# Performance work log

Hardware: AMD Instinct MI355X
Metric: run time of the kernel (lower is better)

Reference implementation:

```python
import jax, jax.numpy as jnp
import numpy as np

EPS = 1e-9
NUM_GATES = 64
SECOND_THRESHOLD = 0.2  # eval threshold (module defaults train==eval)
CAPACITY_FACTOR = 1.25
MIN_EXPERT_CAPACITY = 4


def setup_inputs() -> dict:
    key = jax.random.key(0)
    k1, k2, k3 = jax.random.split(key, 3)
    b, n, d = 8, 2048, 1024
    x = jax.random.normal(k1, (b, n, d), dtype=jnp.float32)
    w_gating = jax.random.normal(k2, (d, NUM_GATES), dtype=jnp.float32)
    uniform_noise = jax.random.uniform(k3, (b, n), dtype=jnp.float32)
    return {"x": x, "w_gating": w_gating, "uniform_noise": uniform_noise}


def reference(x, w_gating, uniform_noise):
    b, n, d = x.shape
    e = NUM_GATES
    dt = x.dtype

    # raw gates: small matmul + softmax over experts
    raw_gates = jax.nn.softmax(jnp.einsum('bnd,de->bne', x, w_gating), axis=-1)

    # top-1 expert
    gate_1 = jnp.max(raw_gates, axis=-1)            # [b, n]
    index_1 = jnp.argmax(raw_gates, axis=-1)        # [b, n]
    mask_1 = jax.nn.one_hot(index_1, e, dtype=dt)   # [b, n, e]
    density_1_proxy = raw_gates

    # top-2 expert (top-1 of gates with top-1 removed)
    gates_wo1 = raw_gates * (1.0 - mask_1)
    gate_2 = jnp.max(gates_wo1, axis=-1)
    index_2 = jnp.argmax(gates_wo1, axis=-1)
    mask_2 = jax.nn.one_hot(index_2, e, dtype=dt)

    # renormalize top-2 gate values
    denom = gate_1 + gate_2 + EPS
    gate_1 = gate_1 / denom
    gate_2 = gate_2 / denom

    # load-balancing loss
    density_1 = jnp.mean(mask_1, axis=-2)                 # [b, e]
    loss = jnp.mean(jnp.mean(density_1_proxy, axis=-2) * density_1) * float(e * e)

    # second policy == 'random': route to 2nd expert with prob ~ gate_2 / threshold
    keep2 = (uniform_noise < (gate_2 / max(SECOND_THRESHOLD, EPS))).astype(dt)
    mask_2 = mask_2 * keep2[..., None]

    # static expert capacity
    cap = max(min(n, int((n * 2) / e * CAPACITY_FACTOR)), MIN_EXPERT_CAPACITY)
    capf = float(cap)

    # exclusive cumsum over tokens -> position of each token within its expert
    pos1 = (jnp.cumsum(mask_1, axis=-2) - mask_1) * mask_1        # [b, n, e]
    mask_1 = mask_1 * (pos1 < capf).astype(dt)
    mask_1_count = jnp.sum(mask_1, axis=-2, keepdims=True)        # [b, 1, e]
    mask_1_flat = jnp.sum(mask_1, axis=-1)                        # [b, n]
    pos1 = jnpp_sum = jnp.sum(pos1, axis=-1)                      # [b, n]
    gate_1 = gate_1 * mask_1_flat

    pos2 = (jnp.cumsum(mask_2, axis=-2) - mask_2) + mask_1_count
    pos2 = pos2 * mask_2
    mask_2 = mask_2 * (pos2 < capf).astype(dt)
    mask_2_flat = jnp.sum(mask_2, axis=-1)
    pos2 = jnp.sum(pos2, axis=-1)
    gate_2 = gate_2 * mask_2_flat

    # combine tensor [b, n, e, cap]; out-of-range positions one-hot to zero
    oh_e1 = jax.nn.one_hot(index_1, e, dtype=dt)
    oh_e2 = jax.nn.one_hot(index_2, e, dtype=dt)
    oh_c1 = jax.nn.one_hot(pos1.astype(jnp.int32), cap, dtype=dt)
    oh_c2 = jax.nn.one_hot(pos2.astype(jnp.int32), cap, dtype=dt)
    combine = (gate_1[..., None, None] * oh_e1[..., :, None] * oh_c1[..., None, :]
               + gate_2[..., None, None] * oh_e2[..., :, None] * oh_c2[..., None, :])
    dispatch = (combine > 0).astype(dt)
    return dispatch, combine, loss
```

## Files before the change

kernel.cpp:

```cpp
#include <hip/hip_runtime.h>
#include <math.h>

#define NTOK 16384
#define NPB  2048
#define DDIM 1024
#define NEXP 64
#define CAP  80
#define ROWF 5120
#define SOUT 83886080LL

typedef float vf4 __attribute__((ext_vector_type(4)));

#define OFF_ROUTE  0
#define OFF_POS1   (OFF_ROUTE + NTOK*4)
#define OFF_POS2   (OFF_POS1  + NTOK*4)
#define OFF_CNT1   (OFF_POS2  + NTOK*4)
#define OFF_PART   (OFF_CNT1  + 2048)
#define OFF_G12    (OFF_PART  + 65536)

__global__ __launch_bounds__(256) void k_gate(
    const float* __restrict__ x, const float* __restrict__ w,
    const float* __restrict__ noise,
    int* __restrict__ route, float2* __restrict__ g12,
    float* __restrict__ part)
{
    __shared__ float xs[32][68];
    __shared__ float wl[32][64];
    __shared__ float lg[64][68];
    __shared__ float sG[4][64];

    const int tid  = threadIdx.x;
    const int tok0 = blockIdx.x * 64;
    const int tx = tid & 15, ty = tid >> 4;
    float acc[4][4] = {{0.f}};

    const float* xb = x + (size_t)tok0 * DDIM;
    const int t0 = tid >> 3, c0 = (tid & 7) * 4;

    float4 px0 = *(const float4*)(xb + (size_t)t0 * DDIM + c0);
    float4 px1 = *(const float4*)(xb + (size_t)(t0 + 32) * DDIM + c0);
    float4 pw0 = ((const float4*)w)[tid];
    float4 pw1 = ((const float4*)w)[tid + 256];

    for (int k0 = 0; k0 < DDIM; k0 += 32) {
        xs[c0+0][t0] = px0.x; xs[c0+1][t0] = px0.y;
        xs[c0+2][t0] = px0.z; xs[c0+3][t0] = px0.w;
        xs[c0+0][t0+32] = px1.x; xs[c0+1][t0+32] = px1.y;
        xs[c0+2][t0+32] = px1.z; xs[c0+3][t0+32] = px1.w;
        ((float4*)wl)[tid]       = pw0;
        ((float4*)wl)[tid + 256] = pw1;
        __syncthreads();

        if (k0 + 32 < DDIM) {
            px0 = *(const float4*)(xb + (size_t)t0 * DDIM + k0 + 32 + c0);
            px1 = *(const float4*)(xb + (size_t)(t0 + 32) * DDIM + k0 + 32 + c0);
            const float4* wp = (const float4*)(w + (size_t)(k0 + 32) * NEXP);
            pw0 = wp[tid];
            pw1 = wp[tid + 256];
        }

        #pragma unroll
        for (int k = 0; k < 32; ++k) {
            float4 a  = *(const float4*)&xs[k][ty * 4];
            float4 bb = *(const float4*)&wl[k][tx * 4];
            float av[4] = {a.x, a.y, a.z, a.w};
            float bv[4] = {bb.x, bb.y, bb.z, bb.w};
            #pragma unroll
            for (int i = 0; i < 4; ++i)
                #pragma unroll
                for (int j = 0; j < 4; ++j)
                    acc[i][j] = fmaf(av[i], bv[j], acc[i][j]);
        }
        __syncthreads();
    }

    #pragma unroll
    for (int i = 0; i < 4; ++i)
        *(float4*)&lg[ty * 4 + i][tx * 4] =
            make_float4(acc[i][0], acc[i][1], acc[i][2], acc[i][3]);
    __syncthreads();

    const int lane = tid & 63;
    const int wv   = tid >> 6;
    float gsum_acc = 0.f;

    for (int it = 0; it < 16; ++it) {
        int t = wv * 16 + it;
        float v = lg[t][lane];

        float m = v; int mi = lane;
        #pragma unroll
        for (int off = 32; off; off >>= 1) {
            float ov = __shfl_xor(m, off, 64);
            int   oi = __shfl_xor(mi, off, 64);
            if (ov > m || (ov == m && oi < mi)) { m = ov; mi = oi; }
        }
        float v2 = (lane == mi) ? -INFINITY : v;
        float m2 = v2; int mi2 = lane;
        #pragma unroll
        for (int off = 32; off; off >>= 1) {
            float ov = __shfl_xor(m2, off, 64);
            int   oi = __shfl_xor(mi2, off, 64);
            if (ov > m2 || (ov == m2 && oi < mi2)) { m2 = ov; mi2 = oi; }
        }
        float ex = expf(v - m);
        float s = ex;
        #pragma unroll
        for (int off = 32; off; off >>= 1) s += __shfl_xor(s, off, 64);

        float inv   = 1.0f / s;
        float gate1 = inv;
        float gate2 = expf(m2 - m) * inv;
        gsum_acc += ex * inv;

        float denom = gate1 + gate2 + 1e-9f;
        float g1n = gate1 / denom;
        float g2n = gate2 / denom;

        int gt = tok0 + t;
        if (lane == 0) {
            float u = noise[gt];
            int k2 = (u < (g2n / 0.2f)) ? 1 : 0;
            route[gt] = mi | (mi2 << 8) | (k2 << 16);
            g12[gt] = make_float2(g1n, g2n);
        }
    }

    sG[wv][lane] = gsum_acc;
    __syncthreads();
    if (tid < 64)
        part[blockIdx.x * 64 + tid] =
            sG[0][tid] + sG[1][tid] + sG[2][tid] + sG[3][tid];
}

__global__ __launch_bounds__(256) void k_pos(
    const int* __restrict__ route,
    int* __restrict__ pos1, int* __restrict__ pos2raw,
    int* __restrict__ cnt1tot)
{
    const int b    = blockIdx.x;
    const int tid  = threadIdx.x;
    const int lane = tid & 63, wv = tid >> 6;
    __shared__ int sr[NPB];
    __shared__ int h1[32][64], h2[32][64];

    for (int i = tid; i < NPB; i += 256) sr[i] = route[b * NPB + i];
    __syncthreads();

    for (int tau = wv; tau < 32; tau += 4) {
        int c1 = 0, c2 = 0;
        const int* p = &sr[tau * 64];
        #pragma unroll 8
        for (int j = 0; j < 64; ++j) {
            int r = p[j];
            c1 += ((r & 255) == lane);
            c2 += ((r >> 16) && (((r >> 8) & 255) == lane));
        }
        h1[tau][lane] = c1; h2[tau][lane] = c2;
    }
    __syncthreads();

    if (tid < 64) {
        int run = 0;
        #pragma unroll 8
        for (int tau = 0; tau < 32; ++tau) {
            int t = h1[tau][tid]; h1[tau][tid] = run; run += t;
        }
        cnt1tot[b * NEXP + tid] = run;
    } else if (tid < 128) {
        int e = tid - 64, run = 0;
        #pragma unroll 8
        for (int tau = 0; tau < 32; ++tau) {
            int t = h2[tau][e]; h2[tau][e] = run; run += t;
        }
    }
    __syncthreads();

    for (int tau = wv; tau < 32; tau += 4) {
        int c1 = h1[tau][lane], c2 = h2[tau][lane];
        const int* p = &sr[tau * 64];
        const int gbase = b * NPB + tau * 64;
        #pragma unroll 4
        for (int j = 0; j < 64; ++j) {
            int r = p[j];
            if ((r & 255) == lane) pos1[gbase + j] = c1++;
            if ((r >> 16) && (((r >> 8) & 255) == lane)) pos2raw[gbase + j] = c2++;
        }
    }
}

__global__ __launch_bounds__(256) void k_out(
    const int* __restrict__ route,
    const int* __restrict__ pos1, const int* __restrict__ pos2raw,
    const int* __restrict__ cnt1tot,
    const float2* __restrict__ g12, const float* __restrict__ part,
    float* __restrict__ out)
{
    const int tid = threadIdx.x;
    const int bid = blockIdx.x;

    if (bid == 4096) {
        __shared__ float red[4];
        float v = 0.f;
        for (int p = tid; p < 512; p += 256) {
            int b = p >> 6, e = p & 63;
            float s = 0.f;
            #pragma unroll 8
            for (int c = 0; c < 32; ++c) s += part[((b << 5) + c) * 64 + e];
            v += s * (float)cnt1tot[p];
        }
        #pragma unroll
        for (int off = 32; off; off >>= 1) v += __shfl_xor(v, off, 64);
        if ((tid & 63) == 0) red[tid >> 6] = v;
        __syncthreads();
        if (tid == 0)
            out[2 * SOUT] = (red[0] + red[1] + red[2] + red[3]) * (1.0f / 524288.0f);
        return;
    }

    const int tg = bid * 4;

    __shared__ int   se[4][2];
    __shared__ float sv[4][2];

    if (tid < 4) {
        int t = tg + tid;
        int b = t >> 11;
        int r  = route[t];
        int i1 = r & 255, i2 = (r >> 8) & 255, k2 = (r >> 16);
        float2 g = g12[t];

        int p1 = pos1[t];
        se[tid][0] = (p1 < CAP) ? (i1 * CAP + p1) : -1;
        sv[tid][0] = g.x;

        int e2 = -1;
        if (k2) {
            int m1c = min(cnt1tot[(b << 6) + i2], CAP);
            int p2  = pos2raw[t] + m1c;
            if (p2 < CAP) e2 = i2 * CAP + p2;
        }
        se[tid][1] = e2;
        sv[tid][1] = g.y;
    }
    __syncthreads();

    vf4* dbase = (vf4*)(out + (size_t)tg * ROWF);
    vf4* cbase = (vf4*)(out + (size_t)SOUT + (size_t)tg * ROWF);
    #pragma unroll
    for (int t = 0; t < 4; ++t) {
        const int   e1 = se[t][0], e2 = se[t][1];
        const float v1 = sv[t][0], v2 = sv[t][1];
        const int   q1 = e1 >> 2, q2 = e2 >> 2;
        vf4* pd = dbase + (size_t)t * (ROWF / 4);
        vf4* pc = cbase + (size_t)t * (ROWF / 4);
        #pragma unroll
        for (int s5 = 0; s5 < 5; ++s5) {
            int s = s5 * 256 + tid;
            vf4 d = {0.f, 0.f, 0.f, 0.f};
            if (s == q1) d[e1 & 3] = 1.f;
            if (s == q2) d[e2 & 3] = 1.f;
            __builtin_nontemporal_store(d, pd + s);
        }
        #pragma unroll
        for (int s5 = 0; s5 < 5; ++s5) {
            int s = s5 * 256 + tid;
            vf4 c = {0.f, 0.f, 0.f, 0.f};
            if (s == q1) c[e1 & 3] = v1;
            if (s == q2) c[e2 & 3] = v2;
            __builtin_nontemporal_store(c, pc + s);
        }
    }
}

extern "C" void kernel_launch(void* const* d_in, const int* in_sizes, int n_in,
                              void* d_out, int out_size, void* d_ws, size_t ws_size,
                              hipStream_t stream) {
    (void)in_sizes; (void)n_in; (void)ws_size; (void)out_size;
    const float* x     = (const float*)d_in[0];
    const float* w     = (const float*)d_in[1];
    const float* noise = (const float*)d_in[2];
    float* out = (float*)d_out;
    char*  ws  = (char*)d_ws;

    int*    route   = (int*)   (ws + OFF_ROUTE);
    int*    pos1    = (int*)   (ws + OFF_POS1);
    int*    pos2raw = (int*)   (ws + OFF_POS2);
    int*    cnt1tot = (int*)   (ws + OFF_CNT1);
    float*  part    = (float*) (ws + OFF_PART);
    float2* g12     = (float2*)(ws + OFF_G12);

    k_gate<<<dim3(NTOK / 64), dim3(256), 0, stream>>>(
        x, w, noise, route, g12, part);
    k_pos<<<dim3(8), dim3(256), 0, stream>>>(
        route, pos1, pos2raw, cnt1tot);
    k_out<<<dim3(4097), dim3(256), 0, stream>>>(
        route, pos1, pos2raw, cnt1tot, g12, part, out);
}
```

Before: 797.6 us.

## Overlap output zero-fill with gating and position kernels, then scatter nonzeros

The dense dispatch/combine output is no longer written in full by the final kernel. Zeroing is split out instead: extra warps in the gating kernel zero the first part of the output, in lockstep with that kernel's barriers, and extra blocks in the position kernel zero the rest. The final kernel then shrinks to one thread per token that writes only the up to two nonzero entries per row. The aim is to hide the memory-bound zero-fill behind the gating matmul and the scan, at the cost of larger blocks in the gating kernel and barrier counts that must match exactly between the zeroing warps and the compute warps.

```diff
diff --git a/kernel.cpp b/kernel.cpp
--- a/kernel.cpp
+++ b/kernel.cpp
@@ -11,6 +11,11 @@
 
 typedef float vf4 __attribute__((ext_vector_type(4)));
 
+#define K1Z_PER_THREAD 192
+#define K1Z_VF4 (256LL * 256 * K1Z_PER_THREAD)
+#define K2Z_BLOCKS 512
+#define K2Z_PER_THREAD 224
+
 #define OFF_ROUTE  0
 #define OFF_POS1   (OFF_ROUTE + NTOK*4)
 #define OFF_POS2   (OFF_POS1  + NTOK*4)
@@ -18,18 +23,38 @@
 #define OFF_PART   (OFF_CNT1  + 2048)
 #define OFF_G12    (OFF_PART  + 65536)
 
-__global__ __launch_bounds__(256) void k_gate(
+__global__ __launch_bounds__(512) void k_gate(
     const float* __restrict__ x, const float* __restrict__ w,
     const float* __restrict__ noise,
     int* __restrict__ route, float2* __restrict__ g12,
-    float* __restrict__ part)
+    float* __restrict__ part, float* __restrict__ out)
 {
     __shared__ float xs[32][68];
     __shared__ float wl[32][64];
     __shared__ float lg[64][68];
     __shared__ float sG[4][64];
 
-    const int tid  = threadIdx.x;
+    const int tid = threadIdx.x;
+
+    if (tid >= 256) {
+        const int zid = tid - 256;
+        vf4 zz = {0.f, 0.f, 0.f, 0.f};
+        vf4* zbase = (vf4*)out + (size_t)blockIdx.x * (256 * K1Z_PER_THREAD) + zid;
+        for (int k0 = 0; k0 < 32; ++k0) {
+            __syncthreads();
+            #pragma unroll
+            for (int m = 0; m < 5; ++m)
+                __builtin_nontemporal_store(zz, zbase + (size_t)(k0 * 5 + m) * 256);
+            __syncthreads();
+        }
+        __syncthreads();
+        #pragma unroll
+        for (int m = 160; m < 192; ++m)
+            __builtin_nontemporal_store(zz, zbase + (size_t)m * 256);
+        __syncthreads();
+        return;
+    }
+
     const int tok0 = blockIdx.x * 64;
     const int tx = tid & 15, ty = tid >> 4;
     float acc[4][4] = {{0.f}};
@@ -136,10 +161,22 @@
 __global__ __launch_bounds__(256) void k_pos(
     const int* __restrict__ route,
     int* __restrict__ pos1, int* __restrict__ pos2raw,
-    int* __restrict__ cnt1tot)
+    int* __restrict__ cnt1tot, float* __restrict__ out)
 {
+    const int tid  = threadIdx.x;
+
+    if (blockIdx.x >= 8) {
+        const int zb = blockIdx.x - 8;
+        vf4 zz = {0.f, 0.f, 0.f, 0.f};
+        vf4* base = (vf4*)out + K1Z_VF4
+                  + (size_t)zb * (256 * K2Z_PER_THREAD) + tid;
+        #pragma unroll 8
+        for (int i = 0; i < K2Z_PER_THREAD; ++i)
+            __builtin_nontemporal_store(zz, base + (size_t)i * 256);
+        return;
+    }
+
     const int b    = blockIdx.x;
-    const int tid  = threadIdx.x;
     const int lane = tid & 63, wv = tid >> 6;
     __shared__ int sr[NPB];
     __shared__ int h1[32][64], h2[32][64];
@@ -199,7 +236,7 @@
     const int tid = threadIdx.x;
     const int bid = blockIdx.x;
 
-    if (bid == 4096) {
+    if (bid == 64) {
         __shared__ float red[4];
         float v = 0.f;
         for (int p = tid; p < 512; p += 256) {
@@ -218,57 +255,26 @@
         return;
     }
 
-    const int tg = bid * 4;
-
-    __shared__ int   se[4][2];
-    __shared__ float sv[4][2];
-
-    if (tid < 4) {
-        int t = tg + tid;
-        int b = t >> 11;
-        int r  = route[t];
-        int i1 = r & 255, i2 = (r >> 8) & 255, k2 = (r >> 16);
-        float2 g = g12[t];
-
-        int p1 = pos1[t];
-        se[tid][0] = (p1 < CAP) ? (i1 * CAP + p1) : -1;
-        sv[tid][0] = g.x;
-
-        int e2 = -1;
-        if (k2) {
-            int m1c = min(cnt1tot[(b << 6) + i2], CAP);
-            int p2  = pos2raw[t] + m1c;
-            if (p2 < CAP) e2 = i2 * CAP + p2;
-        }
-        se[tid][1] = e2;
-        sv[tid][1] = g.y;
-    }
-    __syncthreads();
-
-    vf4* dbase = (vf4*)(out + (size_t)tg * ROWF);
-    vf4* cbase = (vf4*)(out + (size_t)SOUT + (size_t)tg * ROWF);
-    #pragma unroll
-    for (int t = 0; t < 4; ++t) {
-        const int   e1 = se[t][0], e2 = se[t][1];
-        const float v1 = sv[t][0], v2 = sv[t][1];
-        const int   q1 = e1 >> 2, q2 = e2 >> 2;
-        vf4* pd = dbase + (size_t)t * (ROWF / 4);
-        vf4* pc = cbase + (size_t)t * (ROWF / 4);
-        #pragma unroll
-        for (int s5 = 0; s5 < 5; ++s5) {
-            int s = s5 * 256 + tid;
-            vf4 d = {0.f, 0.f, 0.f, 0.f};
-            if (s == q1) d[e1 & 3] = 1.f;
-            if (s == q2) d[e2 & 3] = 1.f;
-            __builtin_nontemporal_store(d, pd + s);
-        }
-        #pragma unroll
-        for (int s5 = 0; s5 < 5; ++s5) {
-            int s = s5 * 256 + tid;
-            vf4 c = {0.f, 0.f, 0.f, 0.f};
-            if (s == q1) c[e1 & 3] = v1;
-            if (s == q2) c[e2 & 3] = v2;
-            __builtin_nontemporal_store(c, pc + s);
+    const int t = bid * 256 + tid;
+    const int b = t >> 11;
+    const int r  = route[t];
+    const int i1 = r & 255, i2 = (r >> 8) & 255, k2 = (r >> 16);
+    const float2 g = g12[t];
+
+    float* drow = out + (size_t)t * ROWF;
+    float* crow = out + (size_t)SOUT + (size_t)t * ROWF;
+
+    const int p1 = pos1[t];
+    if (p1 < CAP) {
+        drow[i1 * CAP + p1] = 1.f;
+        crow[i1 * CAP + p1] = g.x;
+    }
+    if (k2) {
+        int m1c = min(cnt1tot[(b << 6) + i2], CAP);
+        int p2  = pos2raw[t] + m1c;
+        if (p2 < CAP) {
+            drow[i2 * CAP + p2] = 1.f;
+            crow[i2 * CAP + p2] = g.y;
         }
     }
 }
@@ -290,10 +296,10 @@
     float*  part    = (float*) (ws + OFF_PART);
     float2* g12     = (float2*)(ws + OFF_G12);
 
-    k_gate<<<dim3(NTOK / 64), dim3(256), 0, stream>>>(
-        x, w, noise, route, g12, part);
-    k_pos<<<dim3(8), dim3(256), 0, stream>>>(
-        route, pos1, pos2raw, cnt1tot);
-    k_out<<<dim3(4097), dim3(256), 0, stream>>>(
+    k_gate<<<dim3(NTOK / 64), dim3(512), 0, stream>>>(
+        x, w, noise, route, g12, part, out);
+    k_pos<<<dim3(8 + K2Z_BLOCKS), dim3(256), 0, stream>>>(
+        route, pos1, pos2raw, cnt1tot, out);
+    k_out<<<dim3(65), dim3(256), 0, stream>>>(
         route, pos1, pos2raw, cnt1tot, g12, part, out);
 }
```

Result: faster. 758.5 us (-4.9%).
